# Optimization experiments

Hardware: AMD Instinct MI355X
Metric: run time of the kernel (lower is better)

## Reference

```python
import jax, jax.numpy as jnp
import numpy as np

B, T, C, H = 4, 2048, 1024, 16
HD = C // H


def setup_inputs() -> dict:
    key = jax.random.key(0)
    ks = jax.random.split(key, 9)
    s = 1.0 / np.sqrt(C)
    return {
        "x": jax.random.normal(ks[0], (B, T, C), dtype=jnp.float32),
        "Wk": jax.random.uniform(ks[1], (C, C), jnp.float32, -s, s),
        "bk": jax.random.uniform(ks[2], (C,), jnp.float32, -s, s),
        "Wq": jax.random.uniform(ks[3], (C, C), jnp.float32, -s, s),
        "bq": jax.random.uniform(ks[4], (C,), jnp.float32, -s, s),
        "Wv": jax.random.uniform(ks[5], (C, C), jnp.float32, -s, s),
        "bv": jax.random.uniform(ks[6], (C,), jnp.float32, -s, s),
        "Wp": jax.random.uniform(ks[7], (C, C), jnp.float32, -s, s),
        "bp": jax.random.uniform(ks[8], (C,), jnp.float32, -s, s),
        "padding_mask": jnp.ones((B, T), dtype=jnp.int32),
    }


def reference(x, Wk, bk, Wq, bq, Wv, bv, Wp, bp, padding_mask):
    # torch nn.Linear: y = x @ W.T + b  (W is [out, in])
    def split_heads(t):  # [B,T,C] -> [B,H,T,HD]
        return t.reshape(B, T, H, HD).transpose(0, 2, 1, 3)

    k = split_heads(x @ Wk.T + bk)
    q = split_heads(x @ Wq.T + bq)
    v = split_heads(x @ Wv.T + bv)

    scale = 1.0 / jnp.sqrt(jnp.float32(HD))
    att = jnp.einsum("bhqd,bhkd->bhqk", q, k) * scale  # [B,H,T,T]

    causal = jnp.tril(jnp.ones((T, T), dtype=bool))  # [T,T]
    pad = (padding_mask != 0)[:, None, None, :]       # [B,1,1,T]
    mask = causal[None, None, :, :] & pad
    att = jnp.where(mask, att, -jnp.inf)
    att = jax.nn.softmax(att, axis=-1)

    y = jnp.einsum("bhqk,bhkd->bhqd", att, v)  # [B,H,T,HD]
    y = y.transpose(0, 2, 1, 3).reshape(B, T, C)
    return y @ Wp.T + bp
```

## Files before the change

kernel.cpp:

```cpp
#include <hip/hip_runtime.h>
#include <hip/hip_bf16.h>
#include <math.h>
#include <stdint.h>

#define BB 4
#define TT 2048
#define CC 1024
#define HH 16
#define HD 64
#define MM (BB*TT)
#define NQT2 16
#define SCQ 0.180336878f

using f32x2  = __attribute__((ext_vector_type(2))) float;
using f32x4  = __attribute__((ext_vector_type(4))) float;
using f32x16 = __attribute__((ext_vector_type(16))) float;
using i32x4  = __attribute__((ext_vector_type(4))) int;
using bf16x4 = __attribute__((ext_vector_type(4))) __bf16;
using bf16x8 = __attribute__((ext_vector_type(8))) __bf16;

__device__ __forceinline__ float fast_exp2(float x) {
  return __builtin_amdgcn_exp2f(x);
}

__device__ __forceinline__ int cvt_pk_bf16(float lo, float hi_) {
  int r;
  asm("v_cvt_pk_bf16_f32 %0, %1, %2" : "=v"(r) : "v"(lo), "v"(hi_));
  return r;
}

__device__ __forceinline__ f32x2 max2(f32x2 a, f32x2 b) {
  return __builtin_elementwise_max(a, b);
}

__device__ __forceinline__ void gload_lds16(const void* g, void* l) {
  __builtin_amdgcn_global_load_lds(
      (__attribute__((address_space(1))) void*)(void*)(g),
      (__attribute__((address_space(3))) void*)(l), 16, 0, 0);
}

__global__ __launch_bounds__(256)
void cvt_f32_bf16(const float* __restrict__ s, __bf16* __restrict__ d, int n4) {
  int i = blockIdx.x * 256 + threadIdx.x;
  if (i >= n4) return;
  float4 v = ((const float4*)s)[i];
  bf16x4 o;
  o[0] = (__bf16)v.x; o[1] = (__bf16)v.y; o[2] = (__bf16)v.z; o[3] = (__bf16)v.w;
  *(bf16x4*)(d + (size_t)i * 4) = o;
}

__global__ __launch_bounds__(256)
void cvt_w4(const float* __restrict__ Wq, const float* __restrict__ Wk,
            const float* __restrict__ Wv, const float* __restrict__ Wp,
            __bf16* __restrict__ wqkv, __bf16* __restrict__ wpb) {
  int which = blockIdx.y;
  const float* s = which == 0 ? Wq : which == 1 ? Wk : which == 2 ? Wv : Wp;
  __bf16* d = which == 3 ? wpb : wqkv + (size_t)which * CC * CC;
  float sc = which == 0 ? SCQ : 1.f;
  int i = blockIdx.x * 256 + threadIdx.x;
  float4 v = ((const float4*)s)[i];
  bf16x4 o;
  o[0] = (__bf16)(v.x * sc); o[1] = (__bf16)(v.y * sc);
  o[2] = (__bf16)(v.z * sc); o[3] = (__bf16)(v.w * sc);
  *(bf16x4*)(d + (size_t)i * 4) = o;
}

#define WAITV0 asm volatile("s_waitcnt vmcnt(0)" ::: "memory")
#define SB0    __builtin_amdgcn_sched_barrier(0)

__global__ __launch_bounds__(256, 2)
void gemm_qkv(const __bf16* __restrict__ A, const __bf16* __restrict__ Bm,
              const float* __restrict__ b0, const float* __restrict__ b1,
              const float* __restrict__ b2, __bf16* __restrict__ out,
              __bf16* __restrict__ vt) {
  __shared__ __bf16 As[128 * 32];
  __shared__ __bf16 Bs[128 * 32];
  __shared__ __bf16 lt[64 * 130];
  const int tid = threadIdx.x;
  const int wid = tid >> 6, lane = tid & 63;
  const int g = lane >> 4, lq = lane & 15;
  const int bx0 = blockIdx.x;
  const int bx = (bx0 & 7) * 192 + (bx0 >> 3);
  const int bm = bx / 24, bn = bx % 24;
  const int brow = bm << 7, bcol = bn << 7;
  const int wr = (wid >> 1) << 6, wc = (wid & 1) << 6;

  f32x4 acc[4][4] = {};

  const int o0 = wid * 2048 + lane * 16;
  for (int kt = 0; kt < CC; kt += 32) {
    __syncthreads();
#pragma unroll
    for (int j = 0; j < 2; ++j) {
      int o = o0 + j * 1024;
      int row = o >> 6, colb = o & 63;
      gload_lds16((const char*)A + ((size_t)(brow + row) * CC + kt) * 2 + colb,
                  (char*)As + o);
      gload_lds16((const char*)Bm + ((size_t)(bcol + row) * CC + kt) * 2 + colb,
                  (char*)Bs + o);
    }
    __syncthreads();
    bf16x8 av[4], bv[4];
#pragma unroll
    for (int m = 0; m < 4; ++m)
      av[m] = *(const bf16x8*)(As + (wr + m * 16 + lq) * 32 + g * 8);
#pragma unroll
    for (int n = 0; n < 4; ++n)
      bv[n] = *(const bf16x8*)(Bs + (wc + n * 16 + lq) * 32 + g * 8);
#pragma unroll
    for (int m = 0; m < 4; ++m)
#pragma unroll
      for (int n = 0; n < 4; ++n)
        acc[m][n] = __builtin_amdgcn_mfma_f32_16x16x32_bf16(av[m], bv[n], acc[m][n], 0, 0, 0);
  }

  const int proj = bn >> 3;
  if (proj < 2) {
    const float* bias = proj == 0 ? b0 : b1;
    const float bsc = proj == 0 ? SCQ : 1.f;
#pragma unroll
    for (int n = 0; n < 4; ++n) {
      int col = bcol + wc + n * 16 + lq;
      int cw = col & (CC - 1);
      float bb = bias[cw] * bsc;
      int h_ = cw >> 6, d_ = cw & (HD - 1);
#pragma unroll
      for (int m = 0; m < 4; ++m) {
        int row0 = brow + wr + m * 16 + g * 4;
#pragma unroll
        for (int i = 0; i < 4; ++i) {
          int row = row0 + i;
          int b_ = row >> 11, t_ = row & (TT - 1);
          out[((size_t)proj << 23) +
              ((((size_t)b_ * HH + h_) * TT + t_) << 6) + d_] =
              (__bf16)(acc[m][n][i] + bb);
        }
      }
    }
  } else {
    const int cv0 = (bn & 7) << 7;
    const int b_ = brow >> 11, t0 = brow & (TT - 1);
    const int hbase = (bn & 7) << 1;
    const int rd_d = tid >> 2, rd_tb = (tid & 3) << 5;
#pragma unroll
    for (int cc = 0; cc < 2; ++cc) {
      if ((wid & 1) == cc) {
#pragma unroll
        for (int n = 0; n < 4; ++n) {
          int c = (n << 4) + lq;
          float bb = b2[cv0 + (cc << 6) + c];
#pragma unroll
          for (int m = 0; m < 4; ++m) {
            int r = wr + (m << 4) + (g << 2);
            bf16x4 pk;
#pragma unroll
            for (int i = 0; i < 4; ++i)
              pk[i] = (__bf16)(acc[m][n][i] + bb);
            *(bf16x4*)(lt + c * 130 + r) = pk;
          }
        }
      }
      __syncthreads();
      __bf16* dst = vt + (((size_t)((b_ * HH + hbase + cc) * HD + rd_d)) << 11)
                       + t0 + rd_tb;
      const __bf16* srcl = lt + rd_d * 130 + rd_tb;
#pragma unroll
      for (int j = 0; j < 4; ++j)
        *(bf16x8*)(dst + j * 8) = *(const bf16x8*)(srcl + j * 8);
      __syncthreads();
    }
  }
}

__global__ __launch_bounds__(256, 2)
void gemm_proj(const __bf16* __restrict__ A, const __bf16* __restrict__ Bm,
               const float* __restrict__ bias, float* __restrict__ out,
               int M, int N, int K) {
  __shared__ __bf16 As[128 * 32];
  __shared__ __bf16 Bs[128 * 32];
  const int tid = threadIdx.x;
  const int wid = tid >> 6, lane = tid & 63;
  const int g = lane >> 4, lq = lane & 15;
  const int nbn = N >> 7;
  int bx = blockIdx.x;
  const int nb = gridDim.x;
  if ((nb & 7) == 0) { const int q = nb >> 3; bx = (bx & 7) * q + (bx >> 3); }
  const int brow = (bx / nbn) << 7;
  const int bcol = (bx % nbn) << 7;
  const int wr = (wid >> 1) << 6, wc = (wid & 1) << 6;

  f32x4 acc[4][4] = {};

  const int o0 = wid * 2048 + lane * 16;
  for (int kt = 0; kt < K; kt += 32) {
    __syncthreads();
#pragma unroll
    for (int j = 0; j < 2; ++j) {
      int o = o0 + j * 1024;
      int row = o >> 6, colb = o & 63;
      gload_lds16((const char*)A + ((size_t)(brow + row) * K + kt) * 2 + colb,
                  (char*)As + o);
      gload_lds16((const char*)Bm + ((size_t)(bcol + row) * K + kt) * 2 + colb,
                  (char*)Bs + o);
    }
    __syncthreads();
    bf16x8 av[4], bv[4];
#pragma unroll
    for (int m = 0; m < 4; ++m)
      av[m] = *(const bf16x8*)(As + (wr + m * 16 + lq) * 32 + g * 8);
#pragma unroll
    for (int n = 0; n < 4; ++n)
      bv[n] = *(const bf16x8*)(Bs + (wc + n * 16 + lq) * 32 + g * 8);
#pragma unroll
    for (int m = 0; m < 4; ++m)
#pragma unroll
      for (int n = 0; n < 4; ++n)
        acc[m][n] = __builtin_amdgcn_mfma_f32_16x16x32_bf16(av[m], bv[n], acc[m][n], 0, 0, 0);
  }

#pragma unroll
  for (int m = 0; m < 4; ++m) {
#pragma unroll
    for (int n = 0; n < 4; ++n) {
      int col = bcol + wc + n * 16 + lq;
      float bb = bias[col];
      int row0 = brow + wr + m * 16 + g * 4;
#pragma unroll
      for (int i = 0; i < 4; ++i)
        out[(size_t)(row0 + i) * N + col] = acc[m][n][i] + bb;
    }
  }
}

__global__ __launch_bounds__(256, 4)
void attn_fwd(const __bf16* __restrict__ Q, const __bf16* __restrict__ K,
              const __bf16* __restrict__ Vt, const int* __restrict__ pm,
              __bf16* __restrict__ Y) {
  __shared__ __bf16 Ks[2][64 * 64];
  __shared__ __bf16 Vs[2][64 * 64];
  __shared__ int flg;
  const int tid = threadIdx.x, wid = tid >> 6, lane = tid & 63;
  const int l31 = lane & 31, hi = lane >> 5;
  const int bx = blockIdx.x;
  const int bh = bx & 63, jj = bx >> 6;
  const int qi = 15 - (4 * (jj >> 2) + ((jj + (jj >> 2)) & 3));
  const int b_ = bh >> 4, h_ = bh & 15;
  const __bf16* Qb = Q + (size_t)bh * TT * HD;
  const __bf16* Kb = K + (size_t)bh * TT * HD;
  const __bf16* Vb = Vt + (size_t)bh * HD * TT;
  const int* pmb = pm + b_ * TT;

  const int so = tid * 16;
  const int srow = tid >> 3;
  const int scol = (so & 127) ^ ((srow & 7) << 4);

  const int q0 = qi << 7;
  const int qw = q0 + wid * 32;
  const int ntiles = 2 * qi + 2;
  const int sw0 = (l31 & 7) << 4;

  bf16x8 qf[4];
#pragma unroll
  for (int s = 0; s < 4; ++s)
    qf[s] = *(const bf16x8*)(Qb + (size_t)(qw + l31) * HD + s * 16 + hi * 8);
  SB0;

  int4 pa4 = ((const int4*)pmb)[tid];
  int4 pb4 = ((const int4*)pmb)[tid + 256];
  bool okp = pa4.x && pa4.y && pa4.z && pa4.w &&
             pb4.x && pb4.y && pb4.z && pb4.w;
  if (tid == 0) flg = 1;
  __syncthreads();
  if (!okp) flg = 0;

  {
    char* kd = (char*)&Ks[0][0] + so;
    char* vd = (char*)&Vs[0][0] + so;
#pragma unroll
    for (int j = 0; j < 2; ++j) {
      gload_lds16((const char*)Kb + (size_t)(srow + 32 * j) * 128 + scol,
                  kd + j * 4096);
      gload_lds16((const char*)Vb + (size_t)(srow + 32 * j) * (TT * 2) + scol,
                  vd + j * 4096);
    }
  }
  __syncthreads();
  const bool allones = (flg != 0);

  f32x16 o0 = {}, o1 = {};
  f32x16 vzero = {};
  float lsum = 0.f;
  float m = -INFINITY;

  int cur = 0;
#pragma unroll 1
  for (int t = 0; t < ntiles; ++t) {
    const int kv0 = t << 6;
    WAITV0;
    __builtin_amdgcn_s_barrier(); SB0;
    if (t + 1 < ntiles) {
      char* kd = (char*)&Ks[0][0] + (cur ^ 1) * 8192 + so;
      char* vd = (char*)&Vs[0][0] + (cur ^ 1) * 8192 + so;
      const size_t nk = (size_t)(kv0 + 64);
#pragma unroll
      for (int j = 0; j < 2; ++j) {
        gload_lds16((const char*)Kb + (nk + srow + 32 * j) * 128 + scol,
                    kd + j * 4096);
        gload_lds16((const char*)Vb + (size_t)(srow + 32 * j) * (TT * 2) +
                        nk * 2 + scol,
                    vd + j * 4096);
      }
    }

    unsigned long long bits = ~0ull;
    if (__builtin_expect(!allones, 0))
      bits = __ballot(pmb[kv0 + lane] != 0);

    if (kv0 <= qw + 31) {
      const char* VsC = (const char*)&Vs[0][0] + cur * 8192;

#pragma unroll
      for (int h = 0; h < 2; ++h) {
        const int kvh = kv0 + 32 * h;
        if (kvh <= qw + 31) {
          const char* KsC =
              (const char*)&Ks[0][0] + cur * 8192 + (32 * h + l31) * 128;
          f32x16 S;
          __builtin_amdgcn_s_setprio(1);
          {
            bf16x8 k0 = *(const bf16x8*)(KsC + ((16 * hi) ^ sw0));
            S = __builtin_amdgcn_mfma_f32_32x32x16_bf16(k0, qf[0], vzero, 0, 0, 0);
          }
#pragma unroll
          for (int s = 1; s < 4; ++s) {
            bf16x8 kf = *(const bf16x8*)(KsC + ((32 * s + 16 * hi) ^ sw0));
            S = __builtin_amdgcn_mfma_f32_32x32x16_bf16(kf, qf[s], S, 0, 0, 0);
          }
          __builtin_amdgcn_s_setprio(0);

          if (__builtin_expect(bits != ~0ull, 0)) {
#pragma unroll
            for (int r = 0; r < 16; ++r) {
              const int c = (r & 3) + 8 * (r >> 2);
              if (!((bits >> (32 * h + c + 4 * hi)) & 1ull)) S[r] = -INFINITY;
            }
          }
          if (kvh + 31 > qw) {
            const int thr = qw + l31 - kvh - 4 * hi;
#pragma unroll
            for (int r = 0; r < 16; ++r) {
              const int c = (r & 3) + 8 * (r >> 2);
              S[r] = (c <= thr) ? S[r] : -INFINITY;
            }
          }

          f32x2 x0 = {S[0], S[1]},  x1 = {S[2], S[3]};
          f32x2 x2 = {S[4], S[5]},  x3 = {S[6], S[7]};
          f32x2 x4 = {S[8], S[9]},  x5 = {S[10], S[11]};
          f32x2 x6 = {S[12], S[13]}, x7 = {S[14], S[15]};
          x0 = max2(x0, x4); x1 = max2(x1, x5);
          x2 = max2(x2, x6); x3 = max2(x3, x7);
          x0 = max2(x0, x2); x1 = max2(x1, x3);
          x0 = max2(x0, x1);
          float pmax = fmaxf(x0[0], x0[1]);
          if (!__all(pmax <= m + 8.f)) {
            float nm = fmaxf(pmax, __shfl_xor(pmax, 32));
            float mn = fmaxf(m, nm);
            float c = fast_exp2(m - mn);
            m = mn;
            lsum *= c;
#pragma unroll
            for (int r = 0; r < 16; ++r) {
              float cr = __shfl(c, (r & 3) + 8 * (r >> 2) + 4 * hi);
              o0[r] *= cr;
              o1[r] *= cr;
            }
          }

          const f32x2 mm = {m, m};
#pragma unroll
          for (int r = 0; r < 16; r += 2) {
            f32x2 u = {S[r], S[r + 1]};
            u -= mm;
            S[r] = fast_exp2(u[0]);
            S[r + 1] = fast_exp2(u[1]);
          }
          {
            f32x2 u0 = {S[0], S[1]},  u1 = {S[2], S[3]};
            f32x2 u2 = {S[4], S[5]},  u3 = {S[6], S[7]};
            f32x2 u4 = {S[8], S[9]},  u5 = {S[10], S[11]};
            f32x2 u6 = {S[12], S[13]}, u7 = {S[14], S[15]};
            u0 += u4; u1 += u5; u2 += u6; u3 += u7;
            u0 += u2; u1 += u3;
            u0 += u1;
            lsum += u0[0] + u0[1];
          }

          __builtin_amdgcn_s_setprio(1);
#pragma unroll
          for (int s = 0; s < 2; ++s) {
            int A0 = cvt_pk_bf16(S[8 * s + 0], S[8 * s + 1]);
            int A1 = cvt_pk_bf16(S[8 * s + 2], S[8 * s + 3]);
            int B0 = cvt_pk_bf16(S[8 * s + 4], S[8 * s + 5]);
            int B1 = cvt_pk_bf16(S[8 * s + 6], S[8 * s + 7]);
            int s0 = hi ? A0 : B0, s1 = hi ? A1 : B1;
            int e0 = __shfl_xor(s0, 32), e1 = __shfl_xor(s1, 32);
            i32x4 wv;
            wv[0] = hi ? e0 : A0;
            wv[1] = hi ? e1 : A1;
            wv[2] = hi ? B0 : e0;
            wv[3] = hi ? B1 : e1;
            bf16x8 pa = __builtin_bit_cast(bf16x8, wv);
            const int co = 64 * h + 32 * s + 16 * hi;
            bf16x8 v0 = *(const bf16x8*)(VsC + l31 * 128 + (co ^ sw0));
            bf16x8 v1 = *(const bf16x8*)(VsC + (32 + l31) * 128 + (co ^ sw0));
            o0 = __builtin_amdgcn_mfma_f32_32x32x16_bf16(pa, v0, o0, 0, 0, 0);
            o1 = __builtin_amdgcn_mfma_f32_32x32x16_bf16(pa, v1, o1, 0, 0, 0);
          }
          __builtin_amdgcn_s_setprio(0);
        }
      }
    }
    SB0;
    cur ^= 1;
  }

  float linv = 1.f / (lsum + __shfl_xor(lsum, 32));
#pragma unroll
  for (int r = 0; r < 16; ++r) {
    const int crow = (r & 3) + 8 * (r >> 2) + 4 * hi;
    float ir = __shfl(linv, crow);
    const int qrow = qw + crow;
    __bf16* yp = Y + ((size_t)(b_ * TT + qrow)) * CC + h_ * HD + l31;
    yp[0]  = (__bf16)(o0[r] * ir);
    yp[32] = (__bf16)(o1[r] * ir);
  }
}

extern "C" void kernel_launch(void* const* d_in, const int* in_sizes, int n_in,
                              void* d_out, int out_size, void* d_ws, size_t ws_size,
                              hipStream_t stream) {
  (void)in_sizes; (void)n_in; (void)out_size; (void)ws_size;
  const float* x  = (const float*)d_in[0];
  const float* Wk = (const float*)d_in[1];
  const float* bk = (const float*)d_in[2];
  const float* Wq = (const float*)d_in[3];
  const float* bq = (const float*)d_in[4];
  const float* Wv = (const float*)d_in[5];
  const float* bv = (const float*)d_in[6];
  const float* Wp = (const float*)d_in[7];
  const float* bp = (const float*)d_in[8];
  const int* pmask = (const int*)d_in[9];

  char* ws = (char*)d_ws;
  const size_t MB = 1024 * 1024;
  __bf16* xb   = (__bf16*)(ws);
  __bf16* wqkv = (__bf16*)(ws + 16 * MB);
  __bf16* wpb  = (__bf16*)(ws + 22 * MB);
  __bf16* qb   = (__bf16*)(ws + 24 * MB);
  __bf16* kb   = qb + ((size_t)1 << 23);
  __bf16* vtb  = (__bf16*)(ws + 56 * MB);
  __bf16* yb   = xb;

  int n4 = (MM * CC) / 4;
  cvt_f32_bf16<<<(n4 + 255) / 256, 256, 0, stream>>>(x, xb, n4);
  cvt_w4<<<dim3((CC * CC / 4) / 256, 4), 256, 0, stream>>>(
      Wq, Wk, Wv, Wp, wqkv, wpb);

  gemm_qkv<<<(MM / 128) * (3 * CC / 128), 256, 0, stream>>>(
      xb, wqkv, bq, bk, bv, qb, vtb);

  attn_fwd<<<NQT2 * BB * HH, 256, 0, stream>>>(qb, kb, vtb, pmask, yb);

  gemm_proj<<<(MM / 128) * (CC / 128), 256, 0, stream>>>(
      yb, wpb, bp, (float*)d_out, MM, CC, CC);
}
```

Before: 171.9 us.

## Enlarge QKV GEMM tile to 256x128 with 512 threads and swizzled LDS

The QKV projection GEMM now uses a 256x128 block tile with 8 waves (512 threads), so each B tile is reused across twice as many rows. LDS loads and reads use an XOR-style rotation of 16-byte chunks to avoid bank conflicts. The V-transpose epilogue reuses the same shared buffer instead of a separate array. Launch bounds change to (512,6), which may limit registers per thread and risks spills or lower occupancy.

```diff
diff --git a/kernel.cpp b/kernel.cpp
--- a/kernel.cpp
+++ b/kernel.cpp
@@ -68,45 +68,50 @@
 #define WAITV0 asm volatile("s_waitcnt vmcnt(0)" ::: "memory")
 #define SB0    __builtin_amdgcn_sched_barrier(0)
 
-__global__ __launch_bounds__(256, 2)
+__global__ __launch_bounds__(512, 6)
 void gemm_qkv(const __bf16* __restrict__ A, const __bf16* __restrict__ Bm,
               const float* __restrict__ b0, const float* __restrict__ b1,
               const float* __restrict__ b2, __bf16* __restrict__ out,
               __bf16* __restrict__ vt) {
-  __shared__ __bf16 As[128 * 32];
-  __shared__ __bf16 Bs[128 * 32];
-  __shared__ __bf16 lt[64 * 130];
-  const int tid = threadIdx.x;
-  const int wid = tid >> 6, lane = tid & 63;
+  __shared__ __bf16 U[16896];
+  __bf16* As = U;
+  __bf16* Bs = U + 8192;
+  const int tid = threadIdx.x, wid = tid >> 6, lane = tid & 63;
   const int g = lane >> 4, lq = lane & 15;
+  const int wm = wid >> 1, wn = wid & 1;
   const int bx0 = blockIdx.x;
-  const int bx = (bx0 & 7) * 192 + (bx0 >> 3);
+  const int bx = (bx0 & 7) * 96 + (bx0 >> 3);
   const int bm = bx / 24, bn = bx % 24;
-  const int brow = bm << 7, bcol = bn << 7;
-  const int wr = (wid >> 1) << 6, wc = (wid & 1) << 6;
+  const int brow = bm << 8, bcol = bn << 7;
+
+  const int ca = tid, cb = tid + 512;
+  const int ra = ca >> 2, sa_ = (((ca & 3) - (ra >> 1)) & 3) << 4;
+  const int rb = cb >> 2, sb_ = (((cb & 3) - (rb >> 1)) & 3) << 4;
 
   f32x4 acc[4][4] = {};
 
-  const int o0 = wid * 2048 + lane * 16;
   for (int kt = 0; kt < CC; kt += 32) {
     __syncthreads();
-#pragma unroll
-    for (int j = 0; j < 2; ++j) {
-      int o = o0 + j * 1024;
-      int row = o >> 6, colb = o & 63;
-      gload_lds16((const char*)A + ((size_t)(brow + row) * CC + kt) * 2 + colb,
-                  (char*)As + o);
-      gload_lds16((const char*)Bm + ((size_t)(bcol + row) * CC + kt) * 2 + colb,
-                  (char*)Bs + o);
-    }
+    gload_lds16((const char*)A + (size_t)(brow + ra) * 2048 + kt * 2 + sa_,
+                (char*)As + ca * 16);
+    gload_lds16((const char*)A + (size_t)(brow + rb) * 2048 + kt * 2 + sb_,
+                (char*)As + cb * 16);
+    gload_lds16((const char*)Bm + (size_t)(bcol + ra) * 2048 + kt * 2 + sa_,
+                (char*)Bs + ca * 16);
     __syncthreads();
     bf16x8 av[4], bv[4];
 #pragma unroll
-    for (int m = 0; m < 4; ++m)
-      av[m] = *(const bf16x8*)(As + (wr + m * 16 + lq) * 32 + g * 8);
-#pragma unroll
-    for (int n = 0; n < 4; ++n)
-      bv[n] = *(const bf16x8*)(Bs + (wc + n * 16 + lq) * 32 + g * 8);
+    for (int m = 0; m < 4; ++m) {
+      int row = wm * 64 + m * 16 + lq;
+      int sl = (g + (row >> 1)) & 3;
+      av[m] = *(const bf16x8*)((const char*)As + row * 64 + sl * 16);
+    }
+#pragma unroll
+    for (int n = 0; n < 4; ++n) {
+      int row = wn * 64 + n * 16 + lq;
+      int sl = (g + (row >> 1)) & 3;
+      bv[n] = *(const bf16x8*)((const char*)Bs + row * 64 + sl * 16);
+    }
 #pragma unroll
     for (int m = 0; m < 4; ++m)
 #pragma unroll
@@ -120,13 +125,13 @@
     const float bsc = proj == 0 ? SCQ : 1.f;
 #pragma unroll
     for (int n = 0; n < 4; ++n) {
-      int col = bcol + wc + n * 16 + lq;
+      int col = bcol + wn * 64 + n * 16 + lq;
       int cw = col & (CC - 1);
       float bb = bias[cw] * bsc;
       int h_ = cw >> 6, d_ = cw & (HD - 1);
 #pragma unroll
       for (int m = 0; m < 4; ++m) {
-        int row0 = brow + wr + m * 16 + g * 4;
+        int row0 = brow + wm * 64 + m * 16 + g * 4;
 #pragma unroll
         for (int i = 0; i < 4; ++i) {
           int row = row0 + i;
@@ -138,32 +143,34 @@
       }
     }
   } else {
+    __syncthreads();
+    __bf16* lt = U;
     const int cv0 = (bn & 7) << 7;
     const int b_ = brow >> 11, t0 = brow & (TT - 1);
     const int hbase = (bn & 7) << 1;
-    const int rd_d = tid >> 2, rd_tb = (tid & 3) << 5;
+    const int rd_d = tid >> 3, rd_tb = (tid & 7) << 5;
 #pragma unroll
     for (int cc = 0; cc < 2; ++cc) {
-      if ((wid & 1) == cc) {
+      if (wn == cc) {
 #pragma unroll
         for (int n = 0; n < 4; ++n) {
           int c = (n << 4) + lq;
           float bb = b2[cv0 + (cc << 6) + c];
 #pragma unroll
           for (int m = 0; m < 4; ++m) {
-            int r = wr + (m << 4) + (g << 2);
+            int r = wm * 64 + (m << 4) + (g << 2);
             bf16x4 pk;
 #pragma unroll
             for (int i = 0; i < 4; ++i)
               pk[i] = (__bf16)(acc[m][n][i] + bb);
-            *(bf16x4*)(lt + c * 130 + r) = pk;
+            *(bf16x4*)(lt + c * 264 + r) = pk;
           }
         }
       }
       __syncthreads();
       __bf16* dst = vt + (((size_t)((b_ * HH + hbase + cc) * HD + rd_d)) << 11)
                        + t0 + rd_tb;
-      const __bf16* srcl = lt + rd_d * 130 + rd_tb;
+      const __bf16* srcl = lt + rd_d * 264 + rd_tb;
 #pragma unroll
       for (int j = 0; j < 4; ++j)
         *(bf16x8*)(dst + j * 8) = *(const bf16x8*)(srcl + j * 8);
@@ -467,7 +474,7 @@
   cvt_w4<<<dim3((CC * CC / 4) / 256, 4), 256, 0, stream>>>(
       Wq, Wk, Wv, Wp, wqkv, wpb);
 
-  gemm_qkv<<<(MM / 128) * (3 * CC / 128), 256, 0, stream>>>(
+  gemm_qkv<<<(MM / 256) * (3 * CC / 128), 512, 0, stream>>>(
       xb, wqkv, bq, bk, bv, qb, vtb);
 
   attn_fwd<<<NQT2 * BB * HH, 256, 0, stream>>>(qb, kb, vtb, pmask, yb);
```

Result: slower. 475.9 us (+176.8%).
